# Optimization experiments

Hardware: AMD Instinct MI355X
Metric: run time of the kernel (lower is better)

The kernel has to match this reference:

```python
import math
import jax, jax.numpy as jnp
import numpy as np

B, T, D = 4, 2048, 768
NH, DH = 12, 64

def setup_inputs() -> dict:
    key = jax.random.key(0)
    k1, k2, k3 = jax.random.split(key, 3)
    scale_attn = 1.0 / math.sqrt(D)
    scale_proj = 1.0 / math.sqrt(D)
    return {
        "x": jax.random.normal(k1, (B, T, D), dtype=jnp.float32),
        "w_attn": jax.random.normal(k2, (D, 3 * D), dtype=jnp.float32) * scale_attn,
        "b_attn": jnp.zeros((3 * D,), dtype=jnp.float32),
        "w_proj": jax.random.normal(k3, (D, D), dtype=jnp.float32) * scale_proj,
        "b_proj": jnp.zeros((D,), dtype=jnp.float32),
    }

def reference(x, w_attn, b_attn, w_proj, b_proj):
    Bx, Tx, Dx = x.shape
    qkv = x @ w_attn + b_attn                     # [B, T, 3D]
    q, k, v = jnp.split(qkv, 3, axis=-1)          # each [B, T, D]
    # [B, T, D] -> [B, NH, T, DH]
    def to_heads(t):
        return t.reshape(Bx, Tx, NH, DH).transpose(0, 2, 1, 3)
    q, k, v = to_heads(q), to_heads(k), to_heads(v)
    attn = jnp.einsum("bhqd,bhkd->bhqk", q, k) / math.sqrt(DH)
    causal = jnp.tril(jnp.ones((Tx, Tx), dtype=bool))
    attn = jnp.where(causal[None, None, :, :], attn, -jnp.inf)
    attn = jax.nn.softmax(attn, axis=-1)
    out = jnp.einsum("bhqk,bhkd->bhqd", attn, v)  # [B, NH, T, DH]
    out = out.transpose(0, 2, 1, 3).reshape(Bx, Tx, Dx)
    out = out @ w_proj + b_proj
    return (out, (k, v))
```

## Files before the change

kernel.cpp:

```cpp
#include <hip/hip_runtime.h>
#include <hip/hip_bf16.h>

typedef unsigned short ushort_t;
typedef __attribute__((ext_vector_type(8))) short short8;
typedef __attribute__((ext_vector_type(4))) float f32x4;

#define B_    4
#define T_    2048
#define D_    768
#define NH_   12
#define DH_   64
#define KDIM  768

__device__ __forceinline__ ushort_t f2bf(float f) {
  union { float f; unsigned u; } c; c.f = f;
  unsigned u = c.u;
  return (ushort_t)((u + 0x7FFFu + ((u >> 16) & 1u)) >> 16);
}

__device__ __forceinline__ unsigned cvt_pk_bf16(float lo, float hi) {
  unsigned r;
  asm("v_cvt_pk_bf16_f32 %0, %1, %2" : "=v"(r) : "v"(lo), "v"(hi));
  return r;
}

__device__ __forceinline__ void gload_lds16(const void* g, void* l) {
  __builtin_amdgcn_global_load_lds(
      (const __attribute__((address_space(1))) unsigned int*)g,
      (__attribute__((address_space(3))) unsigned int*)l, 16, 0, 0);
}

__global__ void cvt_bf16_vec(const float* __restrict__ in,
                             ushort_t* __restrict__ out, int n4) {
  int i = blockIdx.x * blockDim.x + threadIdx.x;
  if (i >= n4) return;
  float4 v = ((const float4*)in)[i];
  ushort4 o;
  o.x = f2bf(v.x); o.y = f2bf(v.y); o.z = f2bf(v.z); o.w = f2bf(v.w);
  ((ushort4*)out)[i] = o;
}

__global__ void transpose_cvt(const float* __restrict__ in,
                              ushort_t* __restrict__ out, int R, int C) {
  __shared__ float tile[32][33];
  int c0 = blockIdx.x * 32, r0 = blockIdx.y * 32;
  int tx = threadIdx.x, ty = threadIdx.y;
#pragma unroll
  for (int j = 0; j < 32; j += 8)
    tile[ty + j][tx] = in[(size_t)(r0 + ty + j) * C + c0 + tx];
  __syncthreads();
#pragma unroll
  for (int j = 0; j < 32; j += 8)
    out[(size_t)(c0 + ty + j) * R + r0 + tx] = f2bf(tile[tx][ty + j]);
}

__device__ __forceinline__ void gemm128_mainloop(
    const ushort_t* __restrict__ A, const ushort_t* __restrict__ BT,
    int m0, int n0, ushort_t* lds, f32x4 acc[4][4]) {
  const int t = threadIdx.x;
  const int l = t & 63;
  const int w = t >> 6;
  const int wm = w >> 1, wn = w & 1;
  const int c0 = t, c1 = t + 256;
  const ushort_t* ga0 = A + (size_t)(m0 + (c0 >> 2)) * KDIM + ((c0 & 3) << 3);
  const ushort_t* ga1 = A + (size_t)(m0 + (c1 >> 2)) * KDIM + ((c1 & 3) << 3);
  const ushort_t* gb0 = BT + (size_t)(n0 + (c0 >> 2)) * KDIM + ((c0 & 3) << 3);
  const ushort_t* gb1 = BT + (size_t)(n0 + (c1 >> 2)) * KDIM + ((c1 & 3) << 3);
  const int frag_off = ((l & 15) * 32) + ((l >> 4) * 8);
  const int NK = KDIM / 32;

  gload_lds16(ga0, lds + w * 512);
  gload_lds16(ga1, lds + 2048 + w * 512);
  gload_lds16(gb0, lds + 4096 + w * 512);
  gload_lds16(gb1, lds + 6144 + w * 512);
  __syncthreads();

  for (int kk = 0; kk < NK; ++kk) {
    ushort_t* lb = lds + (kk & 1) * 8192;
    if (kk + 1 < NK) {
      ushort_t* ln = lds + ((kk + 1) & 1) * 8192;
      int k0 = (kk + 1) * 32;
      gload_lds16(ga0 + k0, ln + w * 512);
      gload_lds16(ga1 + k0, ln + 2048 + w * 512);
      gload_lds16(gb0 + k0, ln + 4096 + w * 512);
      gload_lds16(gb1 + k0, ln + 6144 + w * 512);
    }
    short8 af[4], bfv[4];
#pragma unroll
    for (int mt = 0; mt < 4; ++mt)
      af[mt] = *(const short8*)&lb[(wm * 64 + mt * 16) * 32 + frag_off];
#pragma unroll
    for (int nt = 0; nt < 4; ++nt)
      bfv[nt] = *(const short8*)&lb[4096 + (wn * 64 + nt * 16) * 32 + frag_off];
#pragma unroll
    for (int mt = 0; mt < 4; ++mt)
#pragma unroll
      for (int nt = 0; nt < 4; ++nt)
        acc[mt][nt] = __builtin_amdgcn_mfma_f32_16x16x32_bf16(
            af[mt], bfv[nt], acc[mt][nt], 0, 0, 0);
    __syncthreads();
  }
}

__global__ __launch_bounds__(256) void gemm_qkv_kernel(
    const ushort_t* __restrict__ xbf, const ushort_t* __restrict__ wT,
    const float* __restrict__ bias, ushort_t* __restrict__ qbf,
    float* __restrict__ kout, float* __restrict__ vout,
    ushort_t* __restrict__ kbf, ushort_t* __restrict__ vtbf) {
  __shared__ ushort_t lds[16384];
  int bid = blockIdx.x;
  int swz = (bid & 7) * 144 + (bid >> 3);
  int m0 = (swz & 63) << 7;
  int n0 = (swz >> 6) << 7;
  f32x4 acc[4][4];
  f32x4 zero = {0.f, 0.f, 0.f, 0.f};
#pragma unroll
  for (int a = 0; a < 4; ++a)
#pragma unroll
    for (int b = 0; b < 4; ++b) acc[a][b] = zero;
  gemm128_mainloop(xbf, wT, m0, n0, lds, acc);

  const float QSC = 0.125f * 1.44269504089f;
  const int l = threadIdx.x & 63, w = threadIdx.x >> 6;
  const int wm = w >> 1, wn = w & 1;
  const int sec = n0 / 768;
  const int b = m0 >> 11;
  const int tt_base = (m0 & 2047) + wm * 64;
#pragma unroll
  for (int nt = 0; nt < 4; ++nt) {
    int n = n0 + wn * 64 + nt * 16 + (l & 15);
    float bv = bias[n];
    int nn = n - sec * 768;
    int h = nn >> 6, dh = nn & 63;
    size_t head_base = ((size_t)(b * NH_ + h) * T_);
#pragma unroll
    for (int mt = 0; mt < 4; ++mt) {
      int tt0 = tt_base + mt * 16 + ((l >> 4) << 2);
      float vals[4];
#pragma unroll
      for (int r = 0; r < 4; ++r) vals[r] = acc[mt][nt][r] + bv;
      if (sec == 0) {
#pragma unroll
        for (int r = 0; r < 4; ++r)
          qbf[((head_base + tt0 + r) << 6) + dh] = f2bf(vals[r] * QSC);
      } else if (sec == 1) {
#pragma unroll
        for (int r = 0; r < 4; ++r) {
          size_t idx = ((head_base + tt0 + r) << 6) + dh;
          kout[idx] = vals[r];
          kbf[idx] = f2bf(vals[r]);
        }
      } else {
#pragma unroll
        for (int r = 0; r < 4; ++r)
          vout[((head_base + tt0 + r) << 6) + dh] = vals[r];
        ushort4 pk;
        pk.x = f2bf(vals[0]); pk.y = f2bf(vals[1]);
        pk.z = f2bf(vals[2]); pk.w = f2bf(vals[3]);
        *(ushort4*)&vtbf[((size_t)(b * NH_ + h) * DH_ + dh) * T_ + tt0] = pk;
      }
    }
  }
}

__global__ __launch_bounds__(256) void gemm_proj_kernel(
    const ushort_t* __restrict__ abf, const ushort_t* __restrict__ wT,
    const float* __restrict__ bias, float* __restrict__ out) {
  __shared__ ushort_t lds[16384];
  int bid = blockIdx.x;
  int swz = (bid & 7) * 48 + (bid >> 3);
  int m0 = (swz & 63) << 7;
  int n0 = (swz >> 6) << 7;
  f32x4 acc[4][4];
  f32x4 zero = {0.f, 0.f, 0.f, 0.f};
#pragma unroll
  for (int a = 0; a < 4; ++a)
#pragma unroll
    for (int b = 0; b < 4; ++b) acc[a][b] = zero;
  gemm128_mainloop(abf, wT, m0, n0, lds, acc);

  const int l = threadIdx.x & 63, w = threadIdx.x >> 6;
  const int wm = w >> 1, wn = w & 1;
#pragma unroll
  for (int nt = 0; nt < 4; ++nt) {
    int n = n0 + wn * 64 + nt * 16 + (l & 15);
    float bv = bias[n];
#pragma unroll
    for (int mt = 0; mt < 4; ++mt) {
#pragma unroll
      for (int r = 0; r < 4; ++r) {
        int m = m0 + wm * 64 + mt * 16 + ((l >> 4) << 2) + r;
        out[(size_t)m * D_ + n] = acc[mt][nt][r] + bv;
      }
    }
  }
}

__device__ __forceinline__ void strip_exp_store(
    f32x4 s4[4], int gq, bool diag, int kvb, int g, int qi, char* pbase) {
  if (diag) {
#pragma unroll
    for (int nt = 0; nt < 4; ++nt)
#pragma unroll
      for (int r = 0; r < 4; ++r) {
        int gk = kvb + nt * 16 + g * 4 + r;
        if (gk > gq) s4[nt][r] = -1e30f;
      }
  }
#pragma unroll
  for (int nt = 0; nt < 4; ++nt) {
    float p0 = exp2f(s4[nt][0]);
    float p1 = exp2f(s4[nt][1]);
    float p2 = exp2f(s4[nt][2]);
    float p3 = exp2f(s4[nt][3]);
    uint2 pk;
    pk.x = cvt_pk_bf16(p0, p1);
    pk.y = cvt_pk_bf16(p2, p3);
    *(uint2*)(pbase + ((nt * 32 + g * 8) ^ ((qi & 7) << 4))) = pk;
  }
}

__global__ __launch_bounds__(256, 4) void attn_fwd_kernel(
    const ushort_t* __restrict__ qbf, const ushort_t* __restrict__ kbf,
    const ushort_t* __restrict__ vtbf, ushort_t* __restrict__ obf) {
  __shared__ ushort_t Kl[2][4096];
  __shared__ ushort_t Vt[2][4096];
  __shared__ ushort_t Pl[4][1024];
  const int bid = blockIdx.x;
  const int swz = (bid & 7) * 96 + (bid >> 3);
  const int jp = swz & 15;
  const int bh = swz >> 4;
  const int qlo = jp << 6, qhi = (31 - jp) << 6;
  const int lastH = 31 - jp, lastL = jp;
  const int t = threadIdx.x, l = t & 63, w = t >> 6;
  const int g = l >> 4, qi = l & 15;

  const ushort_t* Qb = qbf + (size_t)bh * T_ * DH_;
  const ushort_t* Kb = kbf + (size_t)bh * T_ * DH_;
  const ushort_t* Vb = vtbf + (size_t)bh * DH_ * T_;

  const int row0 = t >> 3, ch0 = t & 7, row1 = row0 + 32;
  const ushort_t* gK0 = Kb + row0 * DH_ + ((ch0 ^ (row0 & 7)) << 3);
  const ushort_t* gK1 = Kb + row1 * DH_ + ((ch0 ^ (row1 & 7)) << 3);
  const ushort_t* gV0 = Vb + (size_t)row0 * T_ + ((ch0 ^ (row0 & 7)) << 3);
  const ushort_t* gV1 = Vb + (size_t)row1 * T_ + ((ch0 ^ (row1 & 7)) << 3);

  short8 aqH[2], aqL[2];
  {
    const int qrH = qhi + w * 16 + qi, qrL = qlo + w * 16 + qi;
    aqH[0] = *(const short8*)&Qb[(size_t)qrH * DH_ + (g << 3)];
    aqH[1] = *(const short8*)&Qb[(size_t)qrH * DH_ + (g << 3) + 32];
    aqL[0] = *(const short8*)&Qb[(size_t)qrL * DH_ + (g << 3)];
    aqL[1] = *(const short8*)&Qb[(size_t)qrL * DH_ + (g << 3) + 32];
  }

  short8 ones;
#pragma unroll
  for (int j = 0; j < 8; ++j) ones[j] = (short)0x3F80;

  f32x4 oH[4], oL[4], alH, alL;
  f32x4 zero = {0.f, 0.f, 0.f, 0.f};
#pragma unroll
  for (int nt = 0; nt < 4; ++nt) { oH[nt] = zero; oL[nt] = zero; }
  alH = zero; alL = zero;

  gload_lds16(gK0, &Kl[0][w * 512]);
  gload_lds16(gK1, &Kl[0][2048 + w * 512]);
  gload_lds16(gV0, &Vt[0][w * 512]);
  gload_lds16(gV1, &Vt[0][2048 + w * 512]);
  __syncthreads();

  char* pb = (char*)&Pl[w][0] + qi * 128;

  for (int kt = 0; kt <= lastH; ++kt) {
    const int buf = kt & 1;
    const int kvb = kt << 6;
    if (kt < lastH) {
      const int nx = kt + 1;
      gload_lds16(gK0 + nx * 4096, &Kl[buf ^ 1][w * 512]);
      gload_lds16(gK1 + nx * 4096, &Kl[buf ^ 1][2048 + w * 512]);
      gload_lds16(gV0 + nx * 64, &Vt[buf ^ 1][w * 512]);
      gload_lds16(gV1 + nx * 64, &Vt[buf ^ 1][2048 + w * 512]);
    }
    const bool loAct = (kt <= lastL);

    f32x4 s4H[4], s4L[4];
#pragma unroll
    for (int nt = 0; nt < 4; ++nt) { s4H[nt] = zero; s4L[nt] = zero; }
#pragma unroll
    for (int h2 = 0; h2 < 2; ++h2) {
      short8 bk[4];
#pragma unroll
      for (int nt = 0; nt < 4; ++nt)
        bk[nt] = *(const short8*)&Kl[buf][((nt * 16 + qi) << 6) +
                                          (((g + 4 * h2) ^ (qi & 7)) << 3)];
#pragma unroll
      for (int nt = 0; nt < 4; ++nt)
        s4H[nt] = __builtin_amdgcn_mfma_f32_16x16x32_bf16(bk[nt], aqH[h2],
                                                          s4H[nt], 0, 0, 0);
      if (loAct) {
#pragma unroll
        for (int nt = 0; nt < 4; ++nt)
          s4L[nt] = __builtin_amdgcn_mfma_f32_16x16x32_bf16(bk[nt], aqL[h2],
                                                            s4L[nt], 0, 0, 0);
      }
    }

    strip_exp_store(s4H, qhi + w * 16 + qi, kt == lastH, kvb, g, qi, pb);
#pragma unroll
    for (int k2 = 0; k2 < 2; ++k2) {
      short8 av[4];
#pragma unroll
      for (int nt = 0; nt < 4; ++nt)
        av[nt] = *(const short8*)&Vt[buf][((nt * 16 + qi) << 6) +
                                          (((g + 4 * k2) ^ (qi & 7)) << 3)];
      short8 pf = *(const short8*)(pb + ((g * 16 + k2 * 64) ^ ((qi & 7) << 4)));
#pragma unroll
      for (int nt = 0; nt < 4; ++nt)
        oH[nt] = __builtin_amdgcn_mfma_f32_16x16x32_bf16(av[nt], pf, oH[nt],
                                                         0, 0, 0);
      alH = __builtin_amdgcn_mfma_f32_16x16x32_bf16(ones, pf, alH, 0, 0, 0);
    }

    if (loAct) {
      strip_exp_store(s4L, qlo + w * 16 + qi, kt == lastL, kvb, g, qi, pb);
#pragma unroll
      for (int k2 = 0; k2 < 2; ++k2) {
        short8 av[4];
#pragma unroll
        for (int nt = 0; nt < 4; ++nt)
          av[nt] = *(const short8*)&Vt[buf][((nt * 16 + qi) << 6) +
                                            (((g + 4 * k2) ^ (qi & 7)) << 3)];
        short8 pf = *(const short8*)(pb + ((g * 16 + k2 * 64) ^ ((qi & 7) << 4)));
#pragma unroll
        for (int nt = 0; nt < 4; ++nt)
          oL[nt] = __builtin_amdgcn_mfma_f32_16x16x32_bf16(av[nt], pf, oL[nt],
                                                           0, 0, 0);
        alL = __builtin_amdgcn_mfma_f32_16x16x32_bf16(ones, pf, alL, 0, 0, 0);
      }
    }
    __syncthreads();
  }

  const int b = bh / NH_, h = bh - b * NH_;
#pragma unroll
  for (int s = 0; s < 2; ++s) {
    f32x4* o = s ? oL : oH;
    float inv = 1.f / (s ? alL[0] : alH[0]);
    int qs = (s ? qlo : qhi) + w * 16 + qi;
    size_t rowb = (size_t)(b * T_ + qs) * D_ + h * DH_;
#pragma unroll
    for (int nt = 0; nt < 4; ++nt) {
      ushort4 pk;
      pk.x = f2bf(o[nt][0] * inv);
      pk.y = f2bf(o[nt][1] * inv);
      pk.z = f2bf(o[nt][2] * inv);
      pk.w = f2bf(o[nt][3] * inv);
      *(ushort4*)&obf[rowb + nt * 16 + g * 4] = pk;
    }
  }
}

extern "C" void kernel_launch(void* const* d_in, const int* in_sizes, int n_in,
                              void* d_out, int out_size, void* d_ws, size_t ws_size,
                              hipStream_t stream) {
  const float* x      = (const float*)d_in[0];
  const float* w_attn = (const float*)d_in[1];
  const float* b_attn = (const float*)d_in[2];
  const float* w_proj = (const float*)d_in[3];
  const float* b_proj = (const float*)d_in[4];

  float* out  = (float*)d_out;
  float* kout = out + (size_t)B_ * T_ * D_;
  float* vout = kout + (size_t)B_ * T_ * D_;

  char* ws = (char*)d_ws;
  ushort_t* xbf = (ushort_t*)(ws);
  ushort_t* wTa = (ushort_t*)(ws + 12582912);
  ushort_t* wTp = (ushort_t*)(ws + 16121856);
  ushort_t* qbf = (ushort_t*)(ws + 17301504);
  ushort_t* kbf = (ushort_t*)(ws + 29884416);
  ushort_t* vtbf = (ushort_t*)(ws + 42467328);
  ushort_t* abf = xbf;

  cvt_bf16_vec<<<6144, 256, 0, stream>>>(x, xbf, (B_ * T_ * D_) / 4);
  dim3 tb(32, 8);
  transpose_cvt<<<dim3(72, 24), tb, 0, stream>>>(w_attn, wTa, D_, 3 * D_);
  transpose_cvt<<<dim3(24, 24), tb, 0, stream>>>(w_proj, wTp, D_, D_);

  gemm_qkv_kernel<<<64 * 18, 256, 0, stream>>>(xbf, wTa, b_attn, qbf, kout, vout,
                                               kbf, vtbf);
  attn_fwd_kernel<<<48 * 16, 256, 0, stream>>>(qbf, kbf, vtbf, abf);
  gemm_proj_kernel<<<64 * 6, 256, 0, stream>>>(abf, wTp, b_proj, out);
}
```

Measured before the change: 160.7 us.

## Triple-buffer K in attention and simplify GEMM mainloop to a single buffer

The attention kernel now keeps three K buffers and two V buffers. K is prefetched two tiles ahead and V one tile ahead, and explicit vmcnt waits plus a single barrier per iteration replace the trailing __syncthreads. The occupancy hint drops from 4 to 3 blocks per CU to make room for the extra LDS. Separately, the shared GEMM mainloop loses its double-buffered prefetch and becomes load, sync, compute with half the LDS. Both GEMM kernels also drop their L2-friendly block swizzle. This trades GEMM load/compute overlap and cache locality for deeper attention prefetch and smaller GEMM LDS footprint.

```diff
diff --git a/kernel.cpp b/kernel.cpp
--- a/kernel.cpp
+++ b/kernel.cpp
@@ -66,32 +66,25 @@
   const ushort_t* ga1 = A + (size_t)(m0 + (c1 >> 2)) * KDIM + ((c1 & 3) << 3);
   const ushort_t* gb0 = BT + (size_t)(n0 + (c0 >> 2)) * KDIM + ((c0 & 3) << 3);
   const ushort_t* gb1 = BT + (size_t)(n0 + (c1 >> 2)) * KDIM + ((c1 & 3) << 3);
+  ushort_t* la0 = lds + (0 * 256 + w * 64) * 8;
+  ushort_t* la1 = lds + (1 * 256 + w * 64) * 8;
+  ushort_t* lb0 = lds + 4096 + (0 * 256 + w * 64) * 8;
+  ushort_t* lb1 = lds + 4096 + (1 * 256 + w * 64) * 8;
   const int frag_off = ((l & 15) * 32) + ((l >> 4) * 8);
-  const int NK = KDIM / 32;
-
-  gload_lds16(ga0, lds + w * 512);
-  gload_lds16(ga1, lds + 2048 + w * 512);
-  gload_lds16(gb0, lds + 4096 + w * 512);
-  gload_lds16(gb1, lds + 6144 + w * 512);
-  __syncthreads();
-
-  for (int kk = 0; kk < NK; ++kk) {
-    ushort_t* lb = lds + (kk & 1) * 8192;
-    if (kk + 1 < NK) {
-      ushort_t* ln = lds + ((kk + 1) & 1) * 8192;
-      int k0 = (kk + 1) * 32;
-      gload_lds16(ga0 + k0, ln + w * 512);
-      gload_lds16(ga1 + k0, ln + 2048 + w * 512);
-      gload_lds16(gb0 + k0, ln + 4096 + w * 512);
-      gload_lds16(gb1 + k0, ln + 6144 + w * 512);
-    }
+
+  for (int k0 = 0; k0 < KDIM; k0 += 32) {
+    gload_lds16(ga0 + k0, la0);
+    gload_lds16(ga1 + k0, la1);
+    gload_lds16(gb0 + k0, lb0);
+    gload_lds16(gb1 + k0, lb1);
+    __syncthreads();
     short8 af[4], bfv[4];
 #pragma unroll
     for (int mt = 0; mt < 4; ++mt)
-      af[mt] = *(const short8*)&lb[(wm * 64 + mt * 16) * 32 + frag_off];
+      af[mt] = *(const short8*)&lds[(wm * 64 + mt * 16) * 32 + frag_off];
 #pragma unroll
     for (int nt = 0; nt < 4; ++nt)
-      bfv[nt] = *(const short8*)&lb[4096 + (wn * 64 + nt * 16) * 32 + frag_off];
+      bfv[nt] = *(const short8*)&lds[4096 + (wn * 64 + nt * 16) * 32 + frag_off];
 #pragma unroll
     for (int mt = 0; mt < 4; ++mt)
 #pragma unroll
@@ -107,11 +100,10 @@
     const float* __restrict__ bias, ushort_t* __restrict__ qbf,
     float* __restrict__ kout, float* __restrict__ vout,
     ushort_t* __restrict__ kbf, ushort_t* __restrict__ vtbf) {
-  __shared__ ushort_t lds[16384];
+  __shared__ ushort_t lds[8192];
   int bid = blockIdx.x;
-  int swz = (bid & 7) * 144 + (bid >> 3);
-  int m0 = (swz & 63) << 7;
-  int n0 = (swz >> 6) << 7;
+  int m0 = (bid & 63) << 7;
+  int n0 = (bid >> 6) << 7;
   f32x4 acc[4][4];
   f32x4 zero = {0.f, 0.f, 0.f, 0.f};
 #pragma unroll
@@ -166,11 +158,10 @@
 __global__ __launch_bounds__(256) void gemm_proj_kernel(
     const ushort_t* __restrict__ abf, const ushort_t* __restrict__ wT,
     const float* __restrict__ bias, float* __restrict__ out) {
-  __shared__ ushort_t lds[16384];
+  __shared__ ushort_t lds[8192];
   int bid = blockIdx.x;
-  int swz = (bid & 7) * 48 + (bid >> 3);
-  int m0 = (swz & 63) << 7;
-  int n0 = (swz >> 6) << 7;
+  int m0 = (bid & 63) << 7;
+  int n0 = (bid >> 6) << 7;
   f32x4 acc[4][4];
   f32x4 zero = {0.f, 0.f, 0.f, 0.f};
 #pragma unroll
@@ -220,10 +211,10 @@
   }
 }
 
-__global__ __launch_bounds__(256, 4) void attn_fwd_kernel(
+__global__ __launch_bounds__(256, 3) void attn_fwd_kernel(
     const ushort_t* __restrict__ qbf, const ushort_t* __restrict__ kbf,
     const ushort_t* __restrict__ vtbf, ushort_t* __restrict__ obf) {
-  __shared__ ushort_t Kl[2][4096];
+  __shared__ ushort_t Kl[3][4096];
   __shared__ ushort_t Vt[2][4096];
   __shared__ ushort_t Pl[4][1024];
   const int bid = blockIdx.x;
@@ -268,19 +259,31 @@
   gload_lds16(gK1, &Kl[0][2048 + w * 512]);
   gload_lds16(gV0, &Vt[0][w * 512]);
   gload_lds16(gV1, &Vt[0][2048 + w * 512]);
-  __syncthreads();
+  gload_lds16(gK0 + 4096, &Kl[1][w * 512]);
+  gload_lds16(gK1 + 4096, &Kl[1][2048 + w * 512]);
 
   char* pb = (char*)&Pl[w][0] + qi * 128;
+  int kb = 0;
 
   for (int kt = 0; kt <= lastH; ++kt) {
-    const int buf = kt & 1;
     const int kvb = kt << 6;
+    const int vb = kt & 1;
     if (kt < lastH) {
-      const int nx = kt + 1;
-      gload_lds16(gK0 + nx * 4096, &Kl[buf ^ 1][w * 512]);
-      gload_lds16(gK1 + nx * 4096, &Kl[buf ^ 1][2048 + w * 512]);
-      gload_lds16(gV0 + nx * 64, &Vt[buf ^ 1][w * 512]);
-      gload_lds16(gV1 + nx * 64, &Vt[buf ^ 1][2048 + w * 512]);
+      asm volatile("s_waitcnt vmcnt(2)" ::: "memory");
+    } else {
+      asm volatile("s_waitcnt vmcnt(0)" ::: "memory");
+    }
+    __builtin_amdgcn_sched_barrier(0);
+    __builtin_amdgcn_s_barrier();
+    __builtin_amdgcn_sched_barrier(0);
+    if (kt + 1 <= lastH) {
+      gload_lds16(gV0 + (size_t)(kt + 1) * 64, &Vt[vb ^ 1][w * 512]);
+      gload_lds16(gV1 + (size_t)(kt + 1) * 64, &Vt[vb ^ 1][2048 + w * 512]);
+    }
+    if (kt + 2 <= lastH) {
+      int kb2 = kb + 2 >= 3 ? kb - 1 : kb + 2;
+      gload_lds16(gK0 + (size_t)(kt + 2) * 4096, &Kl[kb2][w * 512]);
+      gload_lds16(gK1 + (size_t)(kt + 2) * 4096, &Kl[kb2][2048 + w * 512]);
     }
     const bool loAct = (kt <= lastL);
 
@@ -292,8 +295,8 @@
       short8 bk[4];
 #pragma unroll
       for (int nt = 0; nt < 4; ++nt)
-        bk[nt] = *(const short8*)&Kl[buf][((nt * 16 + qi) << 6) +
-                                          (((g + 4 * h2) ^ (qi & 7)) << 3)];
+        bk[nt] = *(const short8*)&Kl[kb][((nt * 16 + qi) << 6) +
+                                         (((g + 4 * h2) ^ (qi & 7)) << 3)];
 #pragma unroll
       for (int nt = 0; nt < 4; ++nt)
         s4H[nt] = __builtin_amdgcn_mfma_f32_16x16x32_bf16(bk[nt], aqH[h2],
@@ -312,8 +315,8 @@
       short8 av[4];
 #pragma unroll
       for (int nt = 0; nt < 4; ++nt)
-        av[nt] = *(const short8*)&Vt[buf][((nt * 16 + qi) << 6) +
-                                          (((g + 4 * k2) ^ (qi & 7)) << 3)];
+        av[nt] = *(const short8*)&Vt[vb][((nt * 16 + qi) << 6) +
+                                         (((g + 4 * k2) ^ (qi & 7)) << 3)];
       short8 pf = *(const short8*)(pb + ((g * 16 + k2 * 64) ^ ((qi & 7) << 4)));
 #pragma unroll
       for (int nt = 0; nt < 4; ++nt)
@@ -329,8 +332,8 @@
         short8 av[4];
 #pragma unroll
         for (int nt = 0; nt < 4; ++nt)
-          av[nt] = *(const short8*)&Vt[buf][((nt * 16 + qi) << 6) +
-                                            (((g + 4 * k2) ^ (qi & 7)) << 3)];
+          av[nt] = *(const short8*)&Vt[vb][((nt * 16 + qi) << 6) +
+                                           (((g + 4 * k2) ^ (qi & 7)) << 3)];
         short8 pf = *(const short8*)(pb + ((g * 16 + k2 * 64) ^ ((qi & 7) << 4)));
 #pragma unroll
         for (int nt = 0; nt < 4; ++nt)
@@ -339,7 +342,7 @@
         alL = __builtin_amdgcn_mfma_f32_16x16x32_bf16(ones, pf, alL, 0, 0, 0);
       }
     }
-    __syncthreads();
+    kb = kb + 1 >= 3 ? 0 : kb + 1;
   }
 
   const int b = bh / NH_, h = bh - b * NH_;
```

New measurement: 143.1 us. 10.9% less time.
